# Performance work log

Hardware: AMD Instinct MI355X
Metric: run time of the kernel (lower is better)

## Reference

```python
import jax, jax.numpy as jnp
import numpy as np

N_NODES = 50000
N_EDGES = 800000
K_HOPS = 3


def setup_inputs() -> dict:
    key = jax.random.key(0)
    ks = jax.random.split(key, 8)
    x = jax.random.normal(ks[0], (N_NODES, 56), dtype=jnp.float32)
    edge_index = jax.random.randint(ks[1], (2, N_EDGES), 0, N_NODES, dtype=jnp.int64)
    def glorot(k, shape):
        fan_in, fan_out = shape
        s = (6.0 / (fan_in + fan_out)) ** 0.5
        return jax.random.uniform(k, shape, jnp.float32, -s, s)
    return {
        "x": x,
        "edge_index": edge_index,
        "W1": glorot(ks[2], (56, 64)), "b1": jnp.zeros((64,), jnp.float32),
        "W2": glorot(ks[3], (64, 64)), "b2": jnp.zeros((64,), jnp.float32),
        "W3": glorot(ks[4], (64, 64)), "b3": jnp.zeros((64,), jnp.float32),
        "W4": glorot(ks[5], (64, 256)), "b4": jnp.zeros((256,), jnp.float32),
    }


def _gcn_norm(edge_index, num_nodes, dtype):
    # add self loops (PyG SGConv default), then symmetric D^{-1/2}(A+I)D^{-1/2} weights
    loop = jnp.arange(num_nodes, dtype=edge_index.dtype)
    src = jnp.concatenate([edge_index[0], loop])
    dst = jnp.concatenate([edge_index[1], loop])
    deg = jax.ops.segment_sum(jnp.ones_like(src, dtype=dtype), dst, num_segments=num_nodes)
    dinv = jnp.where(deg > 0, jax.lax.rsqrt(deg), 0.0).astype(dtype)
    norm = dinv[src] * dinv[dst]  # [E + N]
    return src, dst, norm


def _propagate_k(h, src, dst, norm, num_nodes, k):
    # k hops of sparse gather-scale-scatter: h <- A_hat @ h
    for _ in range(k):
        h = jax.ops.segment_sum(h[src] * norm[:, None], dst, num_segments=num_nodes)
    return h


def reference(x, edge_index, W1, b1, W2, b2, W3, b3, W4, b4):
    n = x.shape[0]
    src, dst, norm = _gcn_norm(edge_index, n, x.dtype)
    # SGConv layers (dropout is identity in eval mode)
    h = _propagate_k(x, src, dst, norm, n, K_HOPS) @ W1 + b1
    h = _propagate_k(h, src, dst, norm, n, K_HOPS) @ W2 + b2
    h = _propagate_k(h, src, dst, norm, n, K_HOPS) @ W3 + b3
    return h @ W4 + b4  # [N, output]
```

## Files before the change

### kernel.cpp

```cpp
#include <hip/hip_runtime.h>

#define N_NODES 50000
#define N_EDGES 800000
#define N_GROUPS 12500
#define GSLOTS 128
#define F_IN 56
#define F_PAD 64
#define F_OUT 256
#define NB 32
#define SEG_SZ 6250
#define ZROW N_NODES
#define PAD_E 0x7FFFFFFF


__global__ __launch_bounds__(256) void k_fill(const int* __restrict__ ei,
                                              int* __restrict__ gcnt,
                                              int* __restrict__ ellg) {
  int seg = blockIdx.x & 7;
  int chunk = blockIdx.x >> 3;
  int nchunks = gridDim.x >> 3;
  int stride = nchunks * blockDim.x;
  for (int e = chunk * blockDim.x + threadIdx.x; e < N_EDGES; e += stride) {
    int d = ei[N_EDGES + e];
    if (d / SEG_SZ == seg) {
      int s = ei[e];
      int g = d >> 2;
      int pos = atomicAdd(&gcnt[g], 1);
      ellg[(g << 7) + pos] = (s << 2) | (d & 3);
    }
  }
}


__global__ void k_self(int* __restrict__ gcnt, int* __restrict__ ellg) {
  int i = blockIdx.x * blockDim.x + threadIdx.x;
  if (i >= N_NODES) return;
  int g = i >> 2;
  int pos = atomicAdd(&gcnt[g], 1);
  ellg[(g << 7) + pos] = (i << 2) | (i & 3);
}


__global__ __launch_bounds__(256) void k_sort(const int* __restrict__ gcnt,
                                              int* __restrict__ ellg,
                                              float* __restrict__ dinv,
                                              float* __restrict__ ideg,
                                              float* __restrict__ sqd) {
  int w = (blockIdx.x * blockDim.x + threadIdx.x) >> 6;
  int l = threadIdx.x & 63;
  int cnt = __builtin_amdgcn_readfirstlane(gcnt[w]);
  int* base = ellg + ((size_t)w << 7);
  int v0 = (l < cnt) ? base[l] : PAD_E;
  int v1 = (64 + l < cnt) ? base[64 + l] : PAD_E;

#pragma unroll
  for (int k = 2; k <= 128; k <<= 1) {
#pragma unroll
    for (int j = 64; j > 0; j >>= 1) {
      if (j >= k) continue;
      if (j == 64) {
        int lo = min(v0, v1), hi = max(v0, v1);
        v0 = lo; v1 = hi;
      } else {
        int o0 = __shfl_xor(v0, j);
        int o1 = __shfl_xor(v1, j);
        bool lower = ((l & j) == 0);
        bool up0 = ((l & k) == 0);
        bool up1 = (((l + 64) & k) == 0);
        v0 = (lower == up0) ? min(v0, o0) : max(v0, o0);
        v1 = (lower == up1) ? min(v1, o1) : max(v1, o1);
      }
    }
  }

  int c0 = __popcll(__ballot(v0 != PAD_E && (v0 & 3) == 0)) +
           __popcll(__ballot(v1 != PAD_E && (v1 & 3) == 0));
  int c1 = __popcll(__ballot(v0 != PAD_E && (v0 & 3) == 1)) +
           __popcll(__ballot(v1 != PAD_E && (v1 & 3) == 1));
  int c2 = __popcll(__ballot(v0 != PAD_E && (v0 & 3) == 2)) +
           __popcll(__ballot(v1 != PAD_E && (v1 & 3) == 2));
  int c3 = __popcll(__ballot(v0 != PAD_E && (v0 & 3) == 3)) +
           __popcll(__ballot(v1 != PAD_E && (v1 & 3) == 3));
  if (l < 4) {
    int c = (l == 0) ? c0 : (l == 1) ? c1 : (l == 2) ? c2 : c3;
    float fc = (float)c;
    int node = (w << 2) + l;
    dinv[node] = rsqrtf(fc);
    ideg[node] = 1.0f / fc;
    sqd[node]  = sqrtf(fc);
  }

  base[l] = (v0 == PAD_E) ? (ZROW << 2) : v0;
  base[64 + l] = (v1 == PAD_E) ? (ZROW << 2) : v1;
}


__global__ void k_loadx(const float* __restrict__ x, const float* __restrict__ dinv,
                        float* __restrict__ h) {
  int i = blockIdx.x * blockDim.x + threadIdx.x;
  int nn = i >> 6, f = i & 63;
  float di = dinv[nn];
  float v = 0.f;
  if (f < F_IN) v = x[nn * F_IN + f] * di;
  else if (f == F_IN) v = di;
  h[i] = v;
}


__global__ __launch_bounds__(256) void k_hop(const float* __restrict__ hin,
                                             float* __restrict__ hout,
                                             const int* __restrict__ gcnt,
                                             const int* __restrict__ ellg,
                                             const float* __restrict__ ideg,
                                             float* __restrict__ vsave) {
  int w = (blockIdx.x * blockDim.x + threadIdx.x) >> 6;
  int lane = threadIdx.x & 63;
  int sub = lane >> 4, m = lane & 15, fo = m << 2;
  int cnt = __builtin_amdgcn_readfirstlane(gcnt[w]);
  const int* base = ellg + ((size_t)w << 7);
  int rec0 = base[lane];
  int rec1 = base[64 + lane];
  float4 acc0 = make_float4(0.f, 0.f, 0.f, 0.f);
  float4 acc1 = acc0, acc2 = acc0, acc3 = acc0;
  int nq = (cnt + 3) >> 2;

#define GATHER(IDX, EV, AV)                                          \
  int EV = (IDX < 64) ? __shfl(rec0, IDX) : __shfl(rec1, IDX - 64);  \
  float4 AV = *(const float4*)(hin + (((size_t)(EV >> 2)) << 6) + fo);

#define ACCUM(EV, AV) {                                              \
    int dd = EV & 3;                                                 \
    float m0 = (dd == 0) ? 1.f : 0.f;                                \
    float m1 = (dd == 1) ? 1.f : 0.f;                                \
    float m2 = (dd == 2) ? 1.f : 0.f;                                \
    float m3 = (dd == 3) ? 1.f : 0.f;                                \
    acc0.x = fmaf(m0, AV.x, acc0.x); acc0.y = fmaf(m0, AV.y, acc0.y);\
    acc0.z = fmaf(m0, AV.z, acc0.z); acc0.w = fmaf(m0, AV.w, acc0.w);\
    acc1.x = fmaf(m1, AV.x, acc1.x); acc1.y = fmaf(m1, AV.y, acc1.y);\
    acc1.z = fmaf(m1, AV.z, acc1.z); acc1.w = fmaf(m1, AV.w, acc1.w);\
    acc2.x = fmaf(m2, AV.x, acc2.x); acc2.y = fmaf(m2, AV.y, acc2.y);\
    acc2.z = fmaf(m2, AV.z, acc2.z); acc2.w = fmaf(m2, AV.w, acc2.w);\
    acc3.x = fmaf(m3, AV.x, acc3.x); acc3.y = fmaf(m3, AV.y, acc3.y);\
    acc3.z = fmaf(m3, AV.z, acc3.z); acc3.w = fmaf(m3, AV.w, acc3.w);\
  }

  int g = 0;
  for (; g + 2 <= nq; g += 2) {
    int i0 = (g << 2) + sub;
    int i1 = i0 + 4;
    GATHER(i0, e0, a0)
    GATHER(i1, e1, a1)
    ACCUM(e0, a0)
    ACCUM(e1, a1)
  }
  if (g < nq) {
    int i0 = (g << 2) + sub;
    GATHER(i0, e0, a0)
    ACCUM(e0, a0)
  }
#undef GATHER
#undef ACCUM

#define RED(A) \
  A.x += __shfl_xor(A.x, 16); A.y += __shfl_xor(A.y, 16); \
  A.z += __shfl_xor(A.z, 16); A.w += __shfl_xor(A.w, 16); \
  A.x += __shfl_xor(A.x, 32); A.y += __shfl_xor(A.y, 32); \
  A.z += __shfl_xor(A.z, 32); A.w += __shfl_xor(A.w, 32);
  RED(acc0) RED(acc1) RED(acc2) RED(acc3)
#undef RED

  float4 v = (sub == 0) ? acc0 : (sub == 1) ? acc1 : (sub == 2) ? acc2 : acc3;
  int node = (w << 2) + sub;
  float idg = ideg[node];
  v.x *= idg; v.y *= idg; v.z *= idg; v.w *= idg;
  *(float4*)(hout + (((size_t)node) << 6) + fo) = v;
  if (vsave != nullptr && m == 14) vsave[node] = v.x;
}


__global__ void k_weights(const float* __restrict__ W1, const float* __restrict__ b1,
                          const float* __restrict__ W2, const float* __restrict__ b2,
                          const float* __restrict__ W3, const float* __restrict__ b3,
                          const float* __restrict__ W4, const float* __restrict__ b4,
                          float* __restrict__ Mw, float* __restrict__ c1,
                          float* __restrict__ c2, float* __restrict__ c3) {
  __shared__ float t1[64], t2[64], t3[64];
  int m = blockIdx.x, tid = threadIdx.x;
  if (m < F_IN) {
    if (tid < 64) {
      float a = 0.f;
      for (int k = 0; k < 64; ++k) a = fmaf(W1[m * 64 + k], W2[k * 64 + tid], a);
      t1[tid] = a;
    }
    __syncthreads();
    if (tid < 64) {
      float a = 0.f;
      for (int k = 0; k < 64; ++k) a = fmaf(t1[k], W3[k * 64 + tid], a);
      t2[tid] = a;
    }
    __syncthreads();
    {
      float a = 0.f;
      for (int k = 0; k < 64; ++k) a = fmaf(t2[k], W4[k * 256 + tid], a);
      Mw[m * 256 + tid] = a;
    }
  } else {
    if (tid < 64) {
      float a = 0.f;
      for (int k = 0; k < 64; ++k) a = fmaf(b1[k], W2[k * 64 + tid], a);
      t1[tid] = a;
    }
    __syncthreads();
    if (tid < 64) {
      float a = 0.f, b = 0.f;
      for (int k = 0; k < 64; ++k) {
        float w3 = W3[k * 64 + tid];
        a = fmaf(t1[k], w3, a);
        b = fmaf(b2[k], w3, b);
      }
      t2[tid] = a; t3[tid] = b;
    }
    __syncthreads();
    {
      float a = 0.f, b = 0.f, c = 0.f;
      for (int k = 0; k < 64; ++k) {
        float w4 = W4[k * 256 + tid];
        a = fmaf(t2[k], w4, a);
        b = fmaf(t3[k], w4, b);
        c = fmaf(b3[k], w4, c);
      }
      c1[tid] = a; c2[tid] = b; c3[tid] = c + b4[tid];
    }
  }
}


__global__ __launch_bounds__(256) void k_final(const float* __restrict__ y,
                                               const float* __restrict__ v3u,
                                               const float* __restrict__ v6u,
                                               const float* __restrict__ sqd,
                                               const float* __restrict__ Mw,
                                               const float* __restrict__ c1,
                                               const float* __restrict__ c2,
                                               const float* __restrict__ c3,
                                               float* __restrict__ out) {
  __shared__ float4 yl[NB][16];
  __shared__ float v3l[NB], v6l[NB];
  int tid = threadIdx.x;
  int j = tid;

  float4 Mreg[14];
#pragma unroll
  for (int k4 = 0; k4 < 14; ++k4) {
    Mreg[k4].x = Mw[(k4 * 4 + 0) * F_OUT + j];
    Mreg[k4].y = Mw[(k4 * 4 + 1) * F_OUT + j];
    Mreg[k4].z = Mw[(k4 * 4 + 2) * F_OUT + j];
    Mreg[k4].w = Mw[(k4 * 4 + 3) * F_OUT + j];
  }
  float C1 = c1[j], C2 = c2[j], C3 = c3[j];

  int n0 = blockIdx.x * NB;
  int lim = min(NB, N_NODES - n0);
  for (int i = tid; i < lim * 16; i += 256) {
    int nn = i >> 4, q = i & 15;
    float sq = sqd[n0 + nn];
    float4 v = *(const float4*)(y + ((size_t)(n0 + nn) << 6) + q * 4);
    v.x *= sq; v.y *= sq; v.z *= sq; v.w *= sq;
    yl[nn][q] = v;
  }
  if (tid < lim) {
    float sq = sqd[n0 + tid];
    v3l[tid] = v3u[n0 + tid] * sq;
    v6l[tid] = v6u[n0 + tid] * sq;
  }
  __syncthreads();

  for (int nn = 0; nn < lim; ++nn) {
    float a0 = fmaf(v6l[nn], C1, fmaf(v3l[nn], C2, C3));
    float a1 = 0.f, a2 = 0.f, a3 = 0.f;
#pragma unroll
    for (int k4 = 0; k4 < 14; ++k4) {
      float4 yv = yl[nn][k4];
      a0 = fmaf(yv.x, Mreg[k4].x, a0);
      a1 = fmaf(yv.y, Mreg[k4].y, a1);
      a2 = fmaf(yv.z, Mreg[k4].z, a2);
      a3 = fmaf(yv.w, Mreg[k4].w, a3);
    }
    out[(size_t)(n0 + nn) * F_OUT + j] = (a0 + a1) + (a2 + a3);
  }
}


extern "C" void kernel_launch(void* const* d_in, const int* in_sizes, int n_in,
                              void* d_out, int out_size, void* d_ws, size_t ws_size,
                              hipStream_t stream) {
  const float* x  = (const float*)d_in[0];
  const int*   ei = (const int*)d_in[1];
  const float* W1 = (const float*)d_in[2];
  const float* b1 = (const float*)d_in[3];
  const float* W2 = (const float*)d_in[4];
  const float* b2 = (const float*)d_in[5];
  const float* W3 = (const float*)d_in[6];
  const float* b3 = (const float*)d_in[7];
  const float* W4 = (const float*)d_in[8];
  const float* b4 = (const float*)d_in[9];
  float* out = (float*)d_out;

  char* ws = (char*)d_ws;
  size_t off = 0;
  auto take = [&](size_t bytes) -> void* {
    void* p = ws + off;
    off += (bytes + 255) & ~(size_t)255;
    return p;
  };
  int*   gcnt  = (int*)take((size_t)N_GROUPS * 4);
  float* dinv  = (float*)take((size_t)N_NODES * 4);
  float* ideg  = (float*)take((size_t)N_NODES * 4);
  float* sqd   = (float*)take((size_t)N_NODES * 4);
  float* v3    = (float*)take((size_t)N_NODES * 4);
  float* v6    = (float*)take((size_t)N_NODES * 4);
  int*   ellg  = (int*)take((size_t)N_GROUPS * GSLOTS * 4);
  float* hA    = (float*)take((size_t)(N_NODES + 1) * F_PAD * 4);
  float* hB    = (float*)take((size_t)(N_NODES + 1) * F_PAD * 4);
  float* Mw    = (float*)take((size_t)F_IN * F_OUT * 4);
  float* c1    = (float*)take((size_t)F_OUT * 4);
  float* c2    = (float*)take((size_t)F_OUT * 4);
  float* c3    = (float*)take((size_t)F_OUT * 4);

  (void)hipMemsetAsync(gcnt, 0, (size_t)N_GROUPS * 4, stream);
  (void)hipMemsetAsync(hA + (size_t)ZROW * F_PAD, 0, F_PAD * 4, stream);
  (void)hipMemsetAsync(hB + (size_t)ZROW * F_PAD, 0, F_PAD * 4, stream);
  k_fill<<<1024, 256, 0, stream>>>(ei, gcnt, ellg);
  k_self<<<(N_NODES + 255) / 256, 256, 0, stream>>>(gcnt, ellg);
  k_sort<<<(N_GROUPS * 64) / 256, 256, 0, stream>>>(gcnt, ellg, dinv, ideg, sqd);
  k_loadx<<<(N_NODES * F_PAD) / 256, 256, 0, stream>>>(x, dinv, hA);
  k_weights<<<F_IN + 1, 256, 0, stream>>>(W1, b1, W2, b2, W3, b3, W4, b4, Mw, c1, c2, c3);

  float* src = hA;
  float* dst = hB;
  for (int hop = 1; hop <= 9; ++hop) {
    float* vs = (hop == 3) ? v3 : (hop == 6) ? v6 : nullptr;
    k_hop<<<(N_GROUPS * 64) / 256, 256, 0, stream>>>(src, dst, gcnt, ellg, ideg, vs);
    float* t = src; src = dst; dst = t;
  }
  k_final<<<(N_NODES + NB - 1) / NB, 256, 0, stream>>>(src, v3, v6, sqd, Mw, c1, c2, c3, out);
}
```

Baseline: 357.6 us.

## Process two node groups per wavefront in hop kernel and register-block final GEMM

Each hop wavefront now handles two groups (g and g+6250), walking the second group's quads in reverse order, and the grid is halved. This amortizes launch/wave setup and may improve load balance and latency hiding. The final kernel drops NB to 16 and reorders loops so each thread keeps 16 per-node accumulators in registers, reusing each weight float4 across nodes with unconditional loads that rely on 50000 dividing by 16. The cost is fewer waves for latency hiding in the hop kernel and higher register pressure in the final kernel.

```diff
diff --git a/kernel.cpp b/kernel.cpp
--- a/kernel.cpp
+++ b/kernel.cpp
@@ -3,11 +3,12 @@
 #define N_NODES 50000
 #define N_EDGES 800000
 #define N_GROUPS 12500
+#define HALF_G 6250
 #define GSLOTS 128
 #define F_IN 56
 #define F_PAD 64
 #define F_OUT 256
-#define NB 32
+#define NB 16
 #define SEG_SZ 6250
 #define ZROW N_NODES
 #define PAD_E 0x7FFFFFFF
@@ -107,55 +108,56 @@
 }
 
 
-__global__ __launch_bounds__(256) void k_hop(const float* __restrict__ hin,
-                                             float* __restrict__ hout,
-                                             const int* __restrict__ gcnt,
-                                             const int* __restrict__ ellg,
-                                             const float* __restrict__ ideg,
-                                             float* __restrict__ vsave) {
-  int w = (blockIdx.x * blockDim.x + threadIdx.x) >> 6;
-  int lane = threadIdx.x & 63;
-  int sub = lane >> 4, m = lane & 15, fo = m << 2;
-  int cnt = __builtin_amdgcn_readfirstlane(gcnt[w]);
-  const int* base = ellg + ((size_t)w << 7);
+template<bool ASC>
+__device__ __forceinline__ void hop_group(int g, const float* __restrict__ hin,
+                                          float* __restrict__ hout,
+                                          const int* __restrict__ gcnt,
+                                          const int* __restrict__ ellg,
+                                          const float* __restrict__ ideg,
+                                          float* __restrict__ vsave,
+                                          int lane, int sub, int m, int fo) {
+  int cnt = __builtin_amdgcn_readfirstlane(gcnt[g]);
+  const int* base = ellg + ((size_t)g << 7);
   int rec0 = base[lane];
   int rec1 = base[64 + lane];
   float4 acc0 = make_float4(0.f, 0.f, 0.f, 0.f);
   float4 acc1 = acc0, acc2 = acc0, acc3 = acc0;
   int nq = (cnt + 3) >> 2;
 
-#define GATHER(IDX, EV, AV)                                          \
-  int EV = (IDX < 64) ? __shfl(rec0, IDX) : __shfl(rec1, IDX - 64);  \
+#define GATHER(QI, EV, AV)                                                \
+  int idx_##EV = ((QI) << 2) + sub;                                       \
+  int EV = (idx_##EV < 64) ? __shfl(rec0, idx_##EV)                       \
+                           : __shfl(rec1, idx_##EV - 64);                 \
   float4 AV = *(const float4*)(hin + (((size_t)(EV >> 2)) << 6) + fo);
 
-#define ACCUM(EV, AV) {                                              \
-    int dd = EV & 3;                                                 \
-    float m0 = (dd == 0) ? 1.f : 0.f;                                \
-    float m1 = (dd == 1) ? 1.f : 0.f;                                \
-    float m2 = (dd == 2) ? 1.f : 0.f;                                \
-    float m3 = (dd == 3) ? 1.f : 0.f;                                \
-    acc0.x = fmaf(m0, AV.x, acc0.x); acc0.y = fmaf(m0, AV.y, acc0.y);\
-    acc0.z = fmaf(m0, AV.z, acc0.z); acc0.w = fmaf(m0, AV.w, acc0.w);\
-    acc1.x = fmaf(m1, AV.x, acc1.x); acc1.y = fmaf(m1, AV.y, acc1.y);\
-    acc1.z = fmaf(m1, AV.z, acc1.z); acc1.w = fmaf(m1, AV.w, acc1.w);\
-    acc2.x = fmaf(m2, AV.x, acc2.x); acc2.y = fmaf(m2, AV.y, acc2.y);\
-    acc2.z = fmaf(m2, AV.z, acc2.z); acc2.w = fmaf(m2, AV.w, acc2.w);\
-    acc3.x = fmaf(m3, AV.x, acc3.x); acc3.y = fmaf(m3, AV.y, acc3.y);\
-    acc3.z = fmaf(m3, AV.z, acc3.z); acc3.w = fmaf(m3, AV.w, acc3.w);\
-  }
-
-  int g = 0;
-  for (; g + 2 <= nq; g += 2) {
-    int i0 = (g << 2) + sub;
-    int i1 = i0 + 4;
-    GATHER(i0, e0, a0)
-    GATHER(i1, e1, a1)
+#define ACCUM(EV, AV) {                                                   \
+    int dd = EV & 3;                                                      \
+    float m0 = (dd == 0) ? 1.f : 0.f;                                     \
+    float m1 = (dd == 1) ? 1.f : 0.f;                                     \
+    float m2 = (dd == 2) ? 1.f : 0.f;                                     \
+    float m3 = (dd == 3) ? 1.f : 0.f;                                     \
+    acc0.x = fmaf(m0, AV.x, acc0.x); acc0.y = fmaf(m0, AV.y, acc0.y);     \
+    acc0.z = fmaf(m0, AV.z, acc0.z); acc0.w = fmaf(m0, AV.w, acc0.w);     \
+    acc1.x = fmaf(m1, AV.x, acc1.x); acc1.y = fmaf(m1, AV.y, acc1.y);     \
+    acc1.z = fmaf(m1, AV.z, acc1.z); acc1.w = fmaf(m1, AV.w, acc1.w);     \
+    acc2.x = fmaf(m2, AV.x, acc2.x); acc2.y = fmaf(m2, AV.y, acc2.y);     \
+    acc2.z = fmaf(m2, AV.z, acc2.z); acc2.w = fmaf(m2, AV.w, acc2.w);     \
+    acc3.x = fmaf(m3, AV.x, acc3.x); acc3.y = fmaf(m3, AV.y, acc3.y);     \
+    acc3.z = fmaf(m3, AV.z, acc3.z); acc3.w = fmaf(m3, AV.w, acc3.w);     \
+  }
+
+  int it = 0;
+  for (; it + 2 <= nq; it += 2) {
+    int q0 = ASC ? it : (nq - 1 - it);
+    int q1 = ASC ? (it + 1) : (nq - 2 - it);
+    GATHER(q0, e0, a0)
+    GATHER(q1, e1, a1)
     ACCUM(e0, a0)
     ACCUM(e1, a1)
   }
-  if (g < nq) {
-    int i0 = (g << 2) + sub;
-    GATHER(i0, e0, a0)
+  if (it < nq) {
+    int q0 = ASC ? it : (nq - 1 - it);
+    GATHER(q0, e0, a0)
     ACCUM(e0, a0)
   }
 #undef GATHER
@@ -170,11 +172,25 @@
 #undef RED
 
   float4 v = (sub == 0) ? acc0 : (sub == 1) ? acc1 : (sub == 2) ? acc2 : acc3;
-  int node = (w << 2) + sub;
+  int node = (g << 2) + sub;
   float idg = ideg[node];
   v.x *= idg; v.y *= idg; v.z *= idg; v.w *= idg;
   *(float4*)(hout + (((size_t)node) << 6) + fo) = v;
   if (vsave != nullptr && m == 14) vsave[node] = v.x;
+}
+
+__global__ __launch_bounds__(256) void k_hop(const float* __restrict__ hin,
+                                             float* __restrict__ hout,
+                                             const int* __restrict__ gcnt,
+                                             const int* __restrict__ ellg,
+                                             const float* __restrict__ ideg,
+                                             float* __restrict__ vsave) {
+  int wid = (blockIdx.x * blockDim.x + threadIdx.x) >> 6;
+  int lane = threadIdx.x & 63;
+  if (wid >= HALF_G) return;
+  int sub = lane >> 4, m = lane & 15, fo = m << 2;
+  hop_group<true >(wid, hin, hout, gcnt, ellg, ideg, vsave, lane, sub, m, fo);
+  hop_group<false>(wid + HALF_G, hin, hout, gcnt, ellg, ideg, vsave, lane, sub, m, fo);
 }
 
 
@@ -260,34 +276,42 @@
   float C1 = c1[j], C2 = c2[j], C3 = c3[j];
 
   int n0 = blockIdx.x * NB;
-  int lim = min(NB, N_NODES - n0);
-  for (int i = tid; i < lim * 16; i += 256) {
+  {
+    int i = tid;
     int nn = i >> 4, q = i & 15;
     float sq = sqd[n0 + nn];
     float4 v = *(const float4*)(y + ((size_t)(n0 + nn) << 6) + q * 4);
     v.x *= sq; v.y *= sq; v.z *= sq; v.w *= sq;
     yl[nn][q] = v;
   }
-  if (tid < lim) {
+  if (tid < NB) {
     float sq = sqd[n0 + tid];
     v3l[tid] = v3u[n0 + tid] * sq;
     v6l[tid] = v6u[n0 + tid] * sq;
   }
   __syncthreads();
 
-  for (int nn = 0; nn < lim; ++nn) {
-    float a0 = fmaf(v6l[nn], C1, fmaf(v3l[nn], C2, C3));
-    float a1 = 0.f, a2 = 0.f, a3 = 0.f;
-#pragma unroll
-    for (int k4 = 0; k4 < 14; ++k4) {
+  float acc[NB];
+#pragma unroll
+  for (int nn = 0; nn < NB; ++nn)
+    acc[nn] = fmaf(v6l[nn], C1, fmaf(v3l[nn], C2, C3));
+
+#pragma unroll
+  for (int k4 = 0; k4 < 14; ++k4) {
+    float4 mk = Mreg[k4];
+#pragma unroll
+    for (int nn = 0; nn < NB; ++nn) {
       float4 yv = yl[nn][k4];
-      a0 = fmaf(yv.x, Mreg[k4].x, a0);
-      a1 = fmaf(yv.y, Mreg[k4].y, a1);
-      a2 = fmaf(yv.z, Mreg[k4].z, a2);
-      a3 = fmaf(yv.w, Mreg[k4].w, a3);
-    }
-    out[(size_t)(n0 + nn) * F_OUT + j] = (a0 + a1) + (a2 + a3);
-  }
+      acc[nn] = fmaf(yv.w, mk.w,
+                fmaf(yv.z, mk.z,
+                fmaf(yv.y, mk.y,
+                fmaf(yv.x, mk.x, acc[nn]))));
+    }
+  }
+
+#pragma unroll
+  for (int nn = 0; nn < NB; ++nn)
+    out[(size_t)(n0 + nn) * F_OUT + j] = acc[nn];
 }
 
 
@@ -336,12 +360,13 @@
   k_loadx<<<(N_NODES * F_PAD) / 256, 256, 0, stream>>>(x, dinv, hA);
   k_weights<<<F_IN + 1, 256, 0, stream>>>(W1, b1, W2, b2, W3, b3, W4, b4, Mw, c1, c2, c3);
 
+  int hop_blocks = (HALF_G * 64 + 255) / 256;
   float* src = hA;
   float* dst = hB;
   for (int hop = 1; hop <= 9; ++hop) {
     float* vs = (hop == 3) ? v3 : (hop == 6) ? v6 : nullptr;
-    k_hop<<<(N_GROUPS * 64) / 256, 256, 0, stream>>>(src, dst, gcnt, ellg, ideg, vs);
+    k_hop<<<hop_blocks, 256, 0, stream>>>(src, dst, gcnt, ellg, ideg, vs);
     float* t = src; src = dst; dst = t;
   }
-  k_final<<<(N_NODES + NB - 1) / NB, 256, 0, stream>>>(src, v3, v6, sqd, Mw, c1, c2, c3, out);
-}
+  k_final<<<N_NODES / NB, 256, 0, stream>>>(src, v3, v6, sqd, Mw, c1, c2, c3, out);
+}
```

After: 351.0 us. Within noise of the previous version (-1.9%).
